# Optimization experiments

Measured on AMD Instinct MI355X. Metric: run time of the kernel, lower is better.

Reference implementation:

```python
import jax, jax.numpy as jnp
import numpy as np

DIM = 768
HEADS = 12
HEAD_DIM = DIM // HEADS
MLP_HID = 4 * DIM
DEPTH = 2
BLEND = 0.5
LN_EPS = 1e-5
SCALE = HEAD_DIM ** -0.5

PARAM_NAMES = ['qkv_w', 'qkv_b', 'proj_w', 'proj_b', 'ln1_g', 'ln1_b', 'ln2_g', 'ln2_b', 'mlp_w1', 'mlp_b1', 'mlp_w2', 'mlp_b2']


def setup_inputs() -> dict:
    key = jax.random.key(0)
    keys = jax.random.split(key, 1 + DEPTH * 6)
    inp = {'x': jax.random.normal(keys[0], (4, 1024, DIM), dtype=jnp.float32)}
    ki = 1
    s = 0.02
    for d in range(DEPTH):
        inp[f'qkv_w{d}'] = jax.random.normal(keys[ki], (DIM, 3 * DIM), jnp.float32) * s; ki += 1
        inp[f'qkv_b{d}'] = jnp.zeros((3 * DIM,), jnp.float32)
        inp[f'proj_w{d}'] = jax.random.normal(keys[ki], (DIM, DIM), jnp.float32) * s; ki += 1
        inp[f'proj_b{d}'] = jnp.zeros((DIM,), jnp.float32)
        inp[f'ln1_g{d}'] = jnp.ones((DIM,), jnp.float32)
        inp[f'ln1_b{d}'] = jnp.zeros((DIM,), jnp.float32)
        inp[f'ln2_g{d}'] = jnp.ones((DIM,), jnp.float32)
        inp[f'ln2_b{d}'] = jnp.zeros((DIM,), jnp.float32)
        inp[f'mlp_w1{d}'] = jax.random.normal(keys[ki], (DIM, MLP_HID), jnp.float32) * s; ki += 1
        inp[f'mlp_b1{d}'] = jnp.zeros((MLP_HID,), jnp.float32)
        inp[f'mlp_w2{d}'] = jax.random.normal(keys[ki], (MLP_HID, DIM), jnp.float32) * s; ki += 1
        inp[f'mlp_b2{d}'] = jnp.zeros((DIM,), jnp.float32)
    return inp


def _layernorm(x, g, b):
    mu = jnp.mean(x, axis=-1, keepdims=True)
    var = jnp.mean(jnp.square(x - mu), axis=-1, keepdims=True)
    return (x - mu) * jax.lax.rsqrt(var + LN_EPS) * g + b


def _attention(x, qkv_w, qkv_b, proj_w, proj_b):
    B, N, C = x.shape
    qkv = (x @ qkv_w + qkv_b).reshape(B, N, 3, HEADS, HEAD_DIM)
    qkv = jnp.transpose(qkv, (2, 0, 3, 1, 4))  # [3, B, H, N, hd]
    q, k, v = qkv[0], qkv[1], qkv[2]
    attn = jax.nn.softmax(jnp.einsum('bhnd,bhmd->bhnm', q, k) * SCALE, axis=-1)
    out = jnp.einsum('bhnm,bhmd->bhnd', attn, v)
    out = jnp.transpose(out, (0, 2, 1, 3)).reshape(B, N, C)
    return out @ proj_w + proj_b, attn


def _block(x, params, lvl):
    p = params[lvl]
    h = _layernorm(x, p['ln1_g'], p['ln1_b'])
    x_attn, attn = _attention(h, p['qkv_w'], p['qkv_b'], p['proj_w'], p['proj_b'])
    maps = [attn]
    x = x + x_attn
    if lvl + 1 < DEPTH:
        x_sub, sub_maps = _block(x, params, lvl + 1)
        x = (1.0 - BLEND) * x + BLEND * x_sub
        maps.extend(sub_maps)
    h = _layernorm(x, p['ln2_g'], p['ln2_b'])
    h = jax.nn.gelu(h @ p['mlp_w1'] + p['mlp_b1'], approximate=False) @ p['mlp_w2'] + p['mlp_b2']
    x = x + h
    return x, maps


def reference(x,
              qkv_w0, qkv_b0, proj_w0, proj_b0, ln1_g0, ln1_b0, ln2_g0, ln2_b0, mlp_w10, mlp_b10, mlp_w20, mlp_b20,
              qkv_w1, qkv_b1, proj_w1, proj_b1, ln1_g1, ln1_b1, ln2_g1, ln2_b1, mlp_w11, mlp_b11, mlp_w21, mlp_b21):
    params = [
        dict(qkv_w=qkv_w0, qkv_b=qkv_b0, proj_w=proj_w0, proj_b=proj_b0, ln1_g=ln1_g0, ln1_b=ln1_b0,
             ln2_g=ln2_g0, ln2_b=ln2_b0, mlp_w1=mlp_w10, mlp_b1=mlp_b10, mlp_w2=mlp_w20, mlp_b2=mlp_b20),
        dict(qkv_w=qkv_w1, qkv_b=qkv_b1, proj_w=proj_w1, proj_b=proj_b1, ln1_g=ln1_g1, ln1_b=ln1_b1,
             ln2_g=ln2_g1, ln2_b=ln2_b1, mlp_w1=mlp_w11, mlp_b1=mlp_b11, mlp_w2=mlp_w21, mlp_b2=mlp_b21),
    ]
    out, maps = _block(x, params, 0)
    return (out, *maps)
```

## Files before the change

### kernel.cpp

```cpp
#include <hip/hip_runtime.h>
#include <hip/hip_bf16.h>
#include <stdint.h>

typedef __bf16 bf16;
typedef __bf16 bf16x8 __attribute__((ext_vector_type(8)));
typedef __bf16 bf16x4 __attribute__((ext_vector_type(4)));
typedef float  f32x4  __attribute__((ext_vector_type(4)));

#define GLOAD16(gsrc, ldst)                                                        \
  __builtin_amdgcn_global_load_lds(                                               \
      (const __attribute__((address_space(1))) void*)(gsrc),                      \
      (__attribute__((address_space(3))) void*)(ldst), 16, 0, 0)

__device__ __forceinline__ float gelu_f(float v) {
  return 0.5f * v * (1.0f + erff(v * 0.70710678118654752f));
}

__global__ __launch_bounds__(256) void transpose_all_k(
    const float* __restrict__ qw0, bf16* __restrict__ qt0,
    const float* __restrict__ pw0, bf16* __restrict__ pt0,
    const float* __restrict__ w10, bf16* __restrict__ t10,
    const float* __restrict__ w20, bf16* __restrict__ t20,
    const float* __restrict__ qw1, bf16* __restrict__ qt1,
    const float* __restrict__ pw1, bf16* __restrict__ pt1,
    const float* __restrict__ w11, bf16* __restrict__ t11,
    const float* __restrict__ w21, bf16* __restrict__ t21,
    const float* __restrict__ x, const float* __restrict__ lng,
    const float* __restrict__ lnb, bf16* __restrict__ lnout) {
  int i = blockIdx.x;
  if (i >= 13824) {
    const int token = (i - 13824) * 4 + (threadIdx.x >> 6);
    const int lane  = threadIdx.x & 63;
    const float4* xp = (const float4*)(x + (size_t)token * 768);
    float4 v[3];
    float s = 0.f, ss = 0.f;
#pragma unroll
    for (int j = 0; j < 3; j++) {
      v[j] = xp[lane + j * 64];
      s  += v[j].x + v[j].y + v[j].z + v[j].w;
      ss += v[j].x * v[j].x + v[j].y * v[j].y + v[j].z * v[j].z + v[j].w * v[j].w;
    }
#pragma unroll
    for (int o = 32; o > 0; o >>= 1) { s += __shfl_xor(s, o); ss += __shfl_xor(ss, o); }
    const float mu  = s * (1.f / 768.f);
    const float var = ss * (1.f / 768.f) - mu * mu;
    const float r   = rsqrtf(var + 1e-5f);
#pragma unroll
    for (int j = 0; j < 3; j++) {
      const int c0 = (lane + j * 64) * 4;
      bf16x4 o4;
      o4[0] = (bf16)((v[j].x - mu) * r * lng[c0 + 0] + lnb[c0 + 0]);
      o4[1] = (bf16)((v[j].y - mu) * r * lng[c0 + 1] + lnb[c0 + 1]);
      o4[2] = (bf16)((v[j].z - mu) * r * lng[c0 + 2] + lnb[c0 + 2]);
      o4[3] = (bf16)((v[j].w - mu) * r * lng[c0 + 3] + lnb[c0 + 3]);
      *(bf16x4*)(lnout + (size_t)token * 768 + c0) = o4;
    }
    return;
  }
  __shared__ float tile[32][33];
  const int d = (i >= 6912) ? 1 : 0;
  i -= d * 6912;
  const float* W; bf16* Wt; int K, N, nt;
  if (i < 1728)      { W = d ? qw1 : qw0; Wt = d ? qt1 : qt0; K = 768;  N = 2304; nt = 72; }
  else if (i < 2304) { i -= 1728; W = d ? pw1 : pw0; Wt = d ? pt1 : pt0; K = 768; N = 768; nt = 24; }
  else if (i < 4608) { i -= 2304; W = d ? w11 : w10; Wt = d ? t11 : t10; K = 768; N = 3072; nt = 96; }
  else               { i -= 4608; W = d ? w21 : w20; Wt = d ? t21 : t20; K = 3072; N = 768; nt = 24; }
  const int n0 = (i % nt) * 32, k0 = (i / nt) * 32;
  const int tx = threadIdx.x & 31, ty = threadIdx.x >> 5;
#pragma unroll
  for (int j = ty; j < 32; j += 8)
    tile[j][tx] = W[(size_t)(k0 + j) * N + n0 + tx];
  __syncthreads();
#pragma unroll
  for (int j = ty; j < 32; j += 8)
    Wt[(size_t)(n0 + j) * K + k0 + tx] = (bf16)tile[tx][j];
}

template <int EPI, int NF>
__global__ __launch_bounds__(512, 2) void gemm256_k(
    const bf16* __restrict__ A, int lda,
    const bf16* __restrict__ Bt, int ldb,
    const float* __restrict__ bias,
    void* __restrict__ outp, int ldc, int K, bf16* __restrict__ vtout,
    size_t pstride) {
  extern __shared__ __align__(16) bf16 smem[];
  bf16* As = smem;
  bf16* Bs = smem + 32768;
  const int BROWS = NF * 64;

  const int t = threadIdx.x, wave = t >> 6, lane = t & 63;
  const int g = lane >> 4, l16 = lane & 15;
  const int wm = wave >> 2, wn = wave & 3;
  const int row0 = blockIdx.y * 256, col0 = blockIdx.x * (NF * 64);
  const int koff = (EPI == 4) ? blockIdx.z * K : 0;
  const int KT = K >> 6;

  f32x4 acc[8][NF];
#pragma unroll
  for (int m = 0; m < 8; m++)
#pragma unroll
    for (int n = 0; n < NF; n++) acc[m][n] = f32x4{0.f, 0.f, 0.f, 0.f};

  const int s_r = t >> 3, s_sl = t & 7;

  auto stage = [&](int kt, int tb) {
    const int k0 = koff + (kt << 6);
#pragma unroll
    for (int l = 0; l < 4; ++l) {
      const int row = l * 64 + s_r;
      const int swz = (s_sl ^ (row & 7)) << 3;
      GLOAD16(A + (size_t)(row0 + row) * lda + k0 + swz,
              As + tb * 16384 + row * 64 + (s_sl << 3));
    }
#pragma unroll
    for (int l = 0; l < NF; ++l) {
      const int row = l * 64 + s_r;
      const int swz = (s_sl ^ (row & 7)) << 3;
      GLOAD16(Bt + (size_t)(col0 + row) * ldb + k0 + swz,
              Bs + tb * (BROWS * 64) + row * 64 + (s_sl << 3));
    }
  };

  stage(0, 0);
  __syncthreads();

  for (int j = 0; j < KT; ++j) {
    const int p = j & 1;
    if (j + 1 < KT) stage(j + 1, p ^ 1);

    bf16x8 bfr[NF][2];
#pragma unroll
    for (int n = 0; n < NF; ++n)
#pragma unroll
      for (int kk = 0; kk < 2; ++kk) {
        const int r = wn * (NF * 16) + n * 16 + l16;
        bfr[n][kk] = *(const bf16x8*)(Bs + p * (BROWS * 64) + r * 64 +
                                      ((((kk << 2) + g) ^ (r & 7)) << 3));
      }
#pragma unroll
    for (int quad = 0; quad < 4; ++quad) {
      bf16x8 af[2][2];
#pragma unroll
      for (int mm = 0; mm < 2; ++mm)
#pragma unroll
        for (int kk = 0; kk < 2; ++kk) {
          const int r = wm * 128 + (quad * 2 + mm) * 16 + l16;
          af[mm][kk] = *(const bf16x8*)(As + p * 16384 + r * 64 +
                                        ((((kk << 2) + g) ^ (r & 7)) << 3));
        }
      __builtin_amdgcn_s_barrier();
      __builtin_amdgcn_s_setprio(1);
#pragma unroll
      for (int mm = 0; mm < 2; ++mm)
#pragma unroll
        for (int n = 0; n < NF; ++n)
#pragma unroll
          for (int kk = 0; kk < 2; ++kk)
            acc[quad * 2 + mm][n] = __builtin_amdgcn_mfma_f32_16x16x32_bf16(
                bfr[n][kk], af[mm][kk], acc[quad * 2 + mm][n], 0, 0, 0);
      __builtin_amdgcn_s_setprio(0);
    }
    __syncthreads();
  }

  const int rowb = row0 + wm * 128 + l16;
  const int colb = col0 + wn * (NF * 16) + (g << 2);
  bf16* outb = (bf16*)outp;
  if constexpr (EPI == 4) outb += (size_t)blockIdx.z * pstride;
#pragma unroll
  for (int m = 0; m < 8; ++m) {
    const int row = rowb + m * 16;
#pragma unroll
    for (int n = 0; n < NF; ++n) {
      const int c0 = colb + n * 16;
      f32x4 v = acc[m][n];
      if constexpr (EPI != 4) {
        const float4 b4 = *(const float4*)(bias + c0);
        v[0] += b4.x; v[1] += b4.y; v[2] += b4.z; v[3] += b4.w;
      }
      if constexpr (EPI == 1) {
        v[0] = gelu_f(v[0]); v[1] = gelu_f(v[1]);
        v[2] = gelu_f(v[2]); v[3] = gelu_f(v[3]);
      }
      bf16x4 o4;
      o4[0] = (bf16)v[0]; o4[1] = (bf16)v[1]; o4[2] = (bf16)v[2]; o4[3] = (bf16)v[3];
      *(bf16x4*)(outb + (size_t)row * ldc + c0) = o4;
      if constexpr (EPI == 0) {
        if (c0 >= 1536) {
          const int bq = row >> 10, q = row & 1023;
          const int hd = c0 - 1536, h = hd >> 6, dd = hd & 63;
          bf16* vb = vtout + (size_t)(bq * 12 + h) * 65536 + (size_t)dd * 1024 + q;
          vb[0] = o4[0]; vb[1024] = o4[1]; vb[2048] = o4[2]; vb[3072] = o4[3];
        }
      }
    }
  }
}

template <int NP, int MODE, bool LN>
__global__ __launch_bounds__(256) void reduce_ln_k(
    const bf16* __restrict__ pbuf, const float* __restrict__ bias,
    const float* __restrict__ res, const float* __restrict__ res2,
    float* __restrict__ xout, const float* __restrict__ g,
    const float* __restrict__ b, bf16* __restrict__ lnout) {
  const int token = blockIdx.x * 4 + (threadIdx.x >> 6);
  const int lane  = threadIdx.x & 63;
  float o[12];
  float s = 0.f, ss = 0.f;
#pragma unroll
  for (int j = 0; j < 3; j++) {
    const int c0 = (lane + j * 64) * 4;
    const size_t idx = (size_t)token * 768 + c0;
    const float4 b4 = *(const float4*)(bias + c0);
    float a0 = b4.x, a1 = b4.y, a2 = b4.z, a3 = b4.w;
#pragma unroll
    for (int sp = 0; sp < NP; sp++) {
      const bf16x4 pp = *(const bf16x4*)(pbuf + (size_t)sp * 3145728 + idx);
      a0 += (float)pp[0]; a1 += (float)pp[1]; a2 += (float)pp[2]; a3 += (float)pp[3];
    }
    const float4 r4 = *(const float4*)(res + idx);
    float4 ov;
    if constexpr (MODE == 0) {
      ov.x = a0 + r4.x; ov.y = a1 + r4.y; ov.z = a2 + r4.z; ov.w = a3 + r4.w;
    } else {
      const float4 r2 = *(const float4*)(res2 + idx);
      ov.x = 0.5f * (a0 + r4.x + r2.x); ov.y = 0.5f * (a1 + r4.y + r2.y);
      ov.z = 0.5f * (a2 + r4.z + r2.z); ov.w = 0.5f * (a3 + r4.w + r2.w);
    }
    *(float4*)(xout + idx) = ov;
    o[j * 4 + 0] = ov.x; o[j * 4 + 1] = ov.y; o[j * 4 + 2] = ov.z; o[j * 4 + 3] = ov.w;
    s  += ov.x + ov.y + ov.z + ov.w;
    ss += ov.x * ov.x + ov.y * ov.y + ov.z * ov.z + ov.w * ov.w;
  }
  if constexpr (LN) {
#pragma unroll
    for (int off = 32; off > 0; off >>= 1) { s += __shfl_xor(s, off); ss += __shfl_xor(ss, off); }
    const float mu  = s * (1.f / 768.f);
    const float var = ss * (1.f / 768.f) - mu * mu;
    const float r   = rsqrtf(var + 1e-5f);
#pragma unroll
    for (int j = 0; j < 3; j++) {
      const int c0 = (lane + j * 64) * 4;
      bf16x4 o4;
      o4[0] = (bf16)((o[j * 4 + 0] - mu) * r * g[c0 + 0] + b[c0 + 0]);
      o4[1] = (bf16)((o[j * 4 + 1] - mu) * r * g[c0 + 1] + b[c0 + 1]);
      o4[2] = (bf16)((o[j * 4 + 2] - mu) * r * g[c0 + 2] + b[c0 + 2]);
      o4[3] = (bf16)((o[j * 4 + 3] - mu) * r * g[c0 + 3] + b[c0 + 3]);
      *(bf16x4*)(lnout + (size_t)token * 768 + c0) = o4;
    }
  }
}

__global__ __launch_bounds__(256) void fattn_k(const bf16* __restrict__ qkv,
                                               const bf16* __restrict__ vT,
                                               float* __restrict__ attn,
                                               bf16* __restrict__ aout) {
  __shared__ __align__(16) bf16 Ks[128 * 64];
  __shared__ __align__(16) bf16 Ps[4 * 16 * 128];

  const float S2 = 0.18033688011112042f;

  const int bid = blockIdx.x;
  const int xcd = bid & 7, within = bid >> 3;
  const int bh = xcd * 6 + (within >> 4);
  const int qb = within & 15;
  const int b = bh / 12, h = bh % 12;

  const int t = threadIdx.x, w = t >> 6, lane = t & 63;
  const int g = lane >> 4, l16 = lane & 15;
  const int q0 = qb * 64;

  const bf16* qbp = qkv + (size_t)b * 1024 * 2304 + h * 64;
  const bf16* kbp = qbp + 768;
  const bf16* vt = vT + (size_t)bh * 65536;
  float* Pout = attn + (size_t)bh * 1048576;
  bf16* Pw = Ps + w * 2048;

  bf16x8 qf[2];
#pragma unroll
  for (int kk = 0; kk < 2; kk++)
    qf[kk] = *(const bf16x8*)(qbp + (size_t)(q0 + w * 16 + l16) * 2304 + kk * 32 + g * 8);

  const int kvr = t >> 3, sl = t & 7;

  float l_run = 0.f;

  for (int kv0 = 0; kv0 < 1024; kv0 += 128) {
#pragma unroll
    for (int i = 0; i < 4; i++) {
      const int kvl = i * 32 + kvr;
      GLOAD16(kbp + (size_t)(kv0 + kvl) * 2304 + (sl ^ (kvl & 7)) * 8,
              Ks + i * 2048 + t * 8);
    }
    __syncthreads();
    f32x4 st[8];
#pragma unroll
    for (int mk = 0; mk < 8; mk++) st[mk] = f32x4{0.f, 0.f, 0.f, 0.f};
    __builtin_amdgcn_s_setprio(1);
#pragma unroll
    for (int kk = 0; kk < 2; kk++) {
#pragma unroll
      for (int mk = 0; mk < 8; mk++) {
        const int kv = mk * 16 + l16;
        const bf16x8 kf = *(const bf16x8*)(Ks + ((kv * 64 + kk * 32 + g * 8) ^ ((kv & 7) << 3)));
        st[mk] = __builtin_amdgcn_mfma_f32_16x16x32_bf16(kf, qf[kk], st[mk], 0, 0, 0);
      }
    }
    __builtin_amdgcn_s_setprio(0);
    __syncthreads();
    float sum = 0.f;
#pragma unroll
    for (int mk = 0; mk < 8; mk++)
#pragma unroll
      for (int r = 0; r < 4; r++) sum += exp2f(st[mk][r] * S2);
    sum += __shfl_xor(sum, 16);
    sum += __shfl_xor(sum, 32);
    l_run += sum;
  }

  const float invl = 1.f / l_run;

  f32x4 oacc[4];
#pragma unroll
  for (int nd = 0; nd < 4; nd++) oacc[nd] = f32x4{0.f, 0.f, 0.f, 0.f};

  for (int kv0 = 0; kv0 < 1024; kv0 += 128) {
#pragma unroll
    for (int i = 0; i < 4; i++) {
      const int kvl = i * 32 + kvr;
      GLOAD16(kbp + (size_t)(kv0 + kvl) * 2304 + (sl ^ (kvl & 7)) * 8,
              Ks + i * 2048 + t * 8);
    }
    __syncthreads();
    f32x4 st[8];
#pragma unroll
    for (int mk = 0; mk < 8; mk++) st[mk] = f32x4{0.f, 0.f, 0.f, 0.f};
    __builtin_amdgcn_s_setprio(1);
#pragma unroll
    for (int kk = 0; kk < 2; kk++) {
#pragma unroll
      for (int mk = 0; mk < 8; mk++) {
        const int kv = mk * 16 + l16;
        const bf16x8 kf = *(const bf16x8*)(Ks + ((kv * 64 + kk * 32 + g * 8) ^ ((kv & 7) << 3)));
        st[mk] = __builtin_amdgcn_mfma_f32_16x16x32_bf16(kf, qf[kk], st[mk], 0, 0, 0);
      }
    }
    __builtin_amdgcn_s_setprio(0);
    __syncthreads();

    const int q = q0 + w * 16 + l16;
#pragma unroll
    for (int mk = 0; mk < 8; mk++) {
      f32x4 pv;
      pv[0] = exp2f(st[mk][0] * S2) * invl;
      pv[1] = exp2f(st[mk][1] * S2) * invl;
      pv[2] = exp2f(st[mk][2] * S2) * invl;
      pv[3] = exp2f(st[mk][3] * S2) * invl;
      __builtin_nontemporal_store(pv, (f32x4*)(Pout + (size_t)q * 1024 + kv0 + mk * 16 + g * 4));
      bf16x4 pb;
      pb[0] = (bf16)pv[0]; pb[1] = (bf16)pv[1]; pb[2] = (bf16)pv[2]; pb[3] = (bf16)pv[3];
      *(bf16x4*)(Pw + ((l16 * 128 + mk * 16 + g * 4) ^ ((l16 & 7) << 3))) = pb;
    }

#pragma unroll
    for (int kkv = 0; kkv < 4; kkv++) {
      const bf16x8 pf = *(const bf16x8*)(Pw + ((l16 * 128 + kkv * 32 + g * 8) ^ ((l16 & 7) << 3)));
      bf16x8 vf[4];
#pragma unroll
      for (int nd = 0; nd < 4; nd++)
        vf[nd] = *(const bf16x8*)(vt + (size_t)(nd * 16 + l16) * 1024 + kv0 + kkv * 32 + g * 8);
      __builtin_amdgcn_s_setprio(1);
#pragma unroll
      for (int nd = 0; nd < 4; nd++)
        oacc[nd] = __builtin_amdgcn_mfma_f32_16x16x32_bf16(vf[nd], pf, oacc[nd], 0, 0, 0);
      __builtin_amdgcn_s_setprio(0);
    }
  }

  {
    const int q = q0 + w * 16 + l16;
    bf16* ob = aout + (size_t)(b * 1024 + q) * 768 + h * 64 + g * 4;
#pragma unroll
    for (int nd = 0; nd < 4; nd++) {
      bf16x4 o4;
      o4[0] = (bf16)oacc[nd][0]; o4[1] = (bf16)oacc[nd][1];
      o4[2] = (bf16)oacc[nd][2]; o4[3] = (bf16)oacc[nd][3];
      *(bf16x4*)(ob + nd * 16) = o4;
    }
  }
}

extern "C" void kernel_launch(void* const* d_in, const int* in_sizes, int n_in,
                              void* d_out, int out_size, void* d_ws, size_t ws_size,
                              hipStream_t stream) {
  (void)in_sizes; (void)n_in; (void)out_size; (void)ws_size;
  const float* x = (const float*)d_in[0];
#define IN(d, i) ((const float*)d_in[1 + (d) * 12 + (i)])
  float* outF = (float*)d_out;
  float* attnp[2] = {outF + 3145728, outF + 3145728 + 50331648};

  const int kLds = 114688;
  hipFuncSetAttribute((const void*)gemm256_k<0, 3>,
                      hipFuncAttributeMaxDynamicSharedMemorySize, kLds);
  hipFuncSetAttribute((const void*)gemm256_k<1, 3>,
                      hipFuncAttributeMaxDynamicSharedMemorySize, kLds);
  hipFuncSetAttribute((const void*)gemm256_k<4, 3>,
                      hipFuncAttributeMaxDynamicSharedMemorySize, kLds);

  char* p = (char*)d_ws;
  auto alloc = [&](size_t bytes) { void* r = p; p += bytes; return r; };
  bf16 *qkv_wt[2], *proj_wt[2], *w1t[2], *w2t[2];
  for (int d = 0; d < 2; d++) {
    qkv_wt[d]  = (bf16*)alloc((size_t)2304 * 768 * 2);
    proj_wt[d] = (bf16*)alloc((size_t)768 * 768 * 2);
    w1t[d]     = (bf16*)alloc((size_t)3072 * 768 * 2);
    w2t[d]     = (bf16*)alloc((size_t)768 * 3072 * 2);
  }
  bf16*  hbuf = (bf16*)alloc((size_t)4096 * 768 * 2);
  bf16*  qkvb = (bf16*)alloc((size_t)4096 * 2304 * 2);
  bf16*  pbuf = hbuf;
  bf16*  vT   = (bf16*)alloc((size_t)48 * 64 * 1024 * 2);
  bf16*  aout = (bf16*)alloc((size_t)4096 * 768 * 2);
  bf16*  hid  = (bf16*)alloc((size_t)4096 * 3072 * 2);
  float* xa   = (float*)alloc((size_t)4096 * 768 * 4);
  float* xb   = (float*)alloc((size_t)4096 * 768 * 4);

  transpose_all_k<<<14848, 256, 0, stream>>>(
      IN(0, 0), qkv_wt[0], IN(0, 2), proj_wt[0], IN(0, 8), w1t[0], IN(0, 10), w2t[0],
      IN(1, 0), qkv_wt[1], IN(1, 2), proj_wt[1], IN(1, 8), w1t[1], IN(1, 10), w2t[1],
      x, IN(0, 4), IN(0, 5), hbuf);

  gemm256_k<0, 3><<<dim3(12, 16), 512, kLds, stream>>>(hbuf, 768, qkv_wt[0], 768, IN(0, 1),
                                                       qkvb, 2304, 768, vT, 0);
  fattn_k<<<768, 256, 0, stream>>>(qkvb, vT, attnp[0], aout);
  gemm256_k<4, 3><<<dim3(4, 16, 4), 512, kLds, stream>>>(aout, 768, proj_wt[0], 768, nullptr,
                                                         pbuf, 768, 192, nullptr, 3145728);
  reduce_ln_k<4, 0, true><<<1024, 256, 0, stream>>>(pbuf, IN(0, 3), x, nullptr,
                                                    xa, IN(1, 4), IN(1, 5), hbuf);
  gemm256_k<0, 3><<<dim3(12, 16), 512, kLds, stream>>>(hbuf, 768, qkv_wt[1], 768, IN(1, 1),
                                                       qkvb, 2304, 768, vT, 0);
  fattn_k<<<768, 256, 0, stream>>>(qkvb, vT, attnp[1], aout);
  gemm256_k<4, 3><<<dim3(4, 16, 4), 512, kLds, stream>>>(aout, 768, proj_wt[1], 768, nullptr,
                                                         pbuf, 768, 192, nullptr, 3145728);
  reduce_ln_k<4, 0, true><<<1024, 256, 0, stream>>>(pbuf, IN(1, 3), xa, nullptr,
                                                    xb, IN(1, 6), IN(1, 7), hbuf);
  gemm256_k<1, 3><<<dim3(16, 16), 512, kLds, stream>>>(hbuf, 768, w1t[1], 768, IN(1, 9),
                                                       hid, 3072, 768, nullptr, 0);
  gemm256_k<4, 3><<<dim3(4, 16, 4), 512, kLds, stream>>>(hid, 3072, w2t[1], 3072, nullptr,
                                                         pbuf, 768, 768, nullptr, 3145728);
  reduce_ln_k<4, 1, true><<<1024, 256, 0, stream>>>(pbuf, IN(1, 11), xb, xa,
                                                    xa, IN(0, 6), IN(0, 7), hbuf);
  gemm256_k<1, 3><<<dim3(16, 16), 512, kLds, stream>>>(hbuf, 768, w1t[0], 768, IN(0, 9),
                                                       hid, 3072, 768, nullptr, 0);
  gemm256_k<4, 3><<<dim3(4, 16, 4), 512, kLds, stream>>>(hid, 3072, w2t[0], 3072, nullptr,
                                                         pbuf, 768, 768, nullptr, 3145728);
  reduce_ln_k<4, 0, false><<<1024, 256, 0, stream>>>(pbuf, IN(0, 11), xa, nullptr,
                                                     outF, nullptr, nullptr, nullptr);
#undef IN
}
```

Before: 432.2 us.

## Compute QK^T once, keep unnormalized probabilities in LDS, then write attention map

The attention kernel no longer runs two passes over K (one for the row sums, one for the probabilities). It computes the scores once, stores the unnormalized bf16 exponentials for the whole 64x1024 tile in about 145 KB of dynamic LDS, and then writes the normalized fp32 attention map with coalesced row-wise stores. Blocks grow to 512 threads, with the eight waves split between KV halves for the score stage and head-dim halves for the PV stage, and 1/l is applied to the output at the end. The cost is one workgroup per CU because of the LDS size, and the stored map is now rounded from bf16 values, which loses precision.

```diff
diff --git a/kernel.cpp b/kernel.cpp
--- a/kernel.cpp
+++ b/kernel.cpp
@@ -251,12 +251,14 @@
   }
 }
 
-__global__ __launch_bounds__(256) void fattn_k(const bf16* __restrict__ qkv,
+__global__ __launch_bounds__(512) void fattn_k(const bf16* __restrict__ qkv,
                                                const bf16* __restrict__ vT,
                                                float* __restrict__ attn,
                                                bf16* __restrict__ aout) {
-  __shared__ __align__(16) bf16 Ks[128 * 64];
-  __shared__ __align__(16) bf16 Ps[4 * 16 * 128];
+  extern __shared__ __align__(16) char fsm[];
+  bf16*  Ks = (bf16*)fsm;
+  bf16*  Pl = (bf16*)(fsm + 16384);
+  float* Sr = (float*)(fsm + 16384 + 132096);
 
   const float S2 = 0.18033688011112042f;
 
@@ -268,123 +270,108 @@
 
   const int t = threadIdx.x, w = t >> 6, lane = t & 63;
   const int g = lane >> 4, l16 = lane & 15;
+  const int qg = w & 3, kvh = w >> 2;
   const int q0 = qb * 64;
+  const int qrow = qg * 16 + l16;
 
   const bf16* qbp = qkv + (size_t)b * 1024 * 2304 + h * 64;
   const bf16* kbp = qbp + 768;
   const bf16* vt = vT + (size_t)bh * 65536;
   float* Pout = attn + (size_t)bh * 1048576;
-  bf16* Pw = Ps + w * 2048;
 
   bf16x8 qf[2];
 #pragma unroll
   for (int kk = 0; kk < 2; kk++)
-    qf[kk] = *(const bf16x8*)(qbp + (size_t)(q0 + w * 16 + l16) * 2304 + kk * 32 + g * 8);
+    qf[kk] = *(const bf16x8*)(qbp + (size_t)(q0 + qrow) * 2304 + kk * 32 + g * 8);
 
   const int kvr = t >> 3, sl = t & 7;
-
-  float l_run = 0.f;
+  float psum = 0.f;
 
   for (int kv0 = 0; kv0 < 1024; kv0 += 128) {
 #pragma unroll
-    for (int i = 0; i < 4; i++) {
-      const int kvl = i * 32 + kvr;
+    for (int i = 0; i < 2; i++) {
+      const int kvl = i * 64 + kvr;
       GLOAD16(kbp + (size_t)(kv0 + kvl) * 2304 + (sl ^ (kvl & 7)) * 8,
-              Ks + i * 2048 + t * 8);
+              Ks + i * 4096 + t * 8);
     }
     __syncthreads();
-    f32x4 st[8];
-#pragma unroll
-    for (int mk = 0; mk < 8; mk++) st[mk] = f32x4{0.f, 0.f, 0.f, 0.f};
+    f32x4 st[4];
+#pragma unroll
+    for (int mkf = 0; mkf < 4; mkf++) st[mkf] = f32x4{0.f, 0.f, 0.f, 0.f};
     __builtin_amdgcn_s_setprio(1);
 #pragma unroll
     for (int kk = 0; kk < 2; kk++) {
 #pragma unroll
-      for (int mk = 0; mk < 8; mk++) {
-        const int kv = mk * 16 + l16;
+      for (int mkf = 0; mkf < 4; mkf++) {
+        const int kv = kvh * 64 + mkf * 16 + l16;
         const bf16x8 kf = *(const bf16x8*)(Ks + ((kv * 64 + kk * 32 + g * 8) ^ ((kv & 7) << 3)));
-        st[mk] = __builtin_amdgcn_mfma_f32_16x16x32_bf16(kf, qf[kk], st[mk], 0, 0, 0);
+        st[mkf] = __builtin_amdgcn_mfma_f32_16x16x32_bf16(kf, qf[kk], st[mkf], 0, 0, 0);
       }
     }
     __builtin_amdgcn_s_setprio(0);
-    __syncthreads();
-    float sum = 0.f;
-#pragma unroll
-    for (int mk = 0; mk < 8; mk++)
-#pragma unroll
-      for (int r = 0; r < 4; r++) sum += exp2f(st[mk][r] * S2);
-    sum += __shfl_xor(sum, 16);
-    sum += __shfl_xor(sum, 32);
-    l_run += sum;
-  }
-
-  const float invl = 1.f / l_run;
-
-  f32x4 oacc[4];
-#pragma unroll
-  for (int nd = 0; nd < 4; nd++) oacc[nd] = f32x4{0.f, 0.f, 0.f, 0.f};
-
-  for (int kv0 = 0; kv0 < 1024; kv0 += 128) {
-#pragma unroll
-    for (int i = 0; i < 4; i++) {
-      const int kvl = i * 32 + kvr;
-      GLOAD16(kbp + (size_t)(kv0 + kvl) * 2304 + (sl ^ (kvl & 7)) * 8,
-              Ks + i * 2048 + t * 8);
-    }
-    __syncthreads();
-    f32x4 st[8];
-#pragma unroll
-    for (int mk = 0; mk < 8; mk++) st[mk] = f32x4{0.f, 0.f, 0.f, 0.f};
-    __builtin_amdgcn_s_setprio(1);
-#pragma unroll
-    for (int kk = 0; kk < 2; kk++) {
-#pragma unroll
-      for (int mk = 0; mk < 8; mk++) {
-        const int kv = mk * 16 + l16;
-        const bf16x8 kf = *(const bf16x8*)(Ks + ((kv * 64 + kk * 32 + g * 8) ^ ((kv & 7) << 3)));
-        st[mk] = __builtin_amdgcn_mfma_f32_16x16x32_bf16(kf, qf[kk], st[mk], 0, 0, 0);
-      }
-    }
-    __builtin_amdgcn_s_setprio(0);
-    __syncthreads();
-
-    const int q = q0 + w * 16 + l16;
-#pragma unroll
-    for (int mk = 0; mk < 8; mk++) {
+#pragma unroll
+    for (int mkf = 0; mkf < 4; mkf++) {
       f32x4 pv;
-      pv[0] = exp2f(st[mk][0] * S2) * invl;
-      pv[1] = exp2f(st[mk][1] * S2) * invl;
-      pv[2] = exp2f(st[mk][2] * S2) * invl;
-      pv[3] = exp2f(st[mk][3] * S2) * invl;
-      __builtin_nontemporal_store(pv, (f32x4*)(Pout + (size_t)q * 1024 + kv0 + mk * 16 + g * 4));
+      pv[0] = exp2f(st[mkf][0] * S2);
+      pv[1] = exp2f(st[mkf][1] * S2);
+      pv[2] = exp2f(st[mkf][2] * S2);
+      pv[3] = exp2f(st[mkf][3] * S2);
+      psum += pv[0] + pv[1] + pv[2] + pv[3];
       bf16x4 pb;
       pb[0] = (bf16)pv[0]; pb[1] = (bf16)pv[1]; pb[2] = (bf16)pv[2]; pb[3] = (bf16)pv[3];
-      *(bf16x4*)(Pw + ((l16 * 128 + mk * 16 + g * 4) ^ ((l16 & 7) << 3))) = pb;
-    }
-
-#pragma unroll
-    for (int kkv = 0; kkv < 4; kkv++) {
-      const bf16x8 pf = *(const bf16x8*)(Pw + ((l16 * 128 + kkv * 32 + g * 8) ^ ((l16 & 7) << 3)));
-      bf16x8 vf[4];
-#pragma unroll
-      for (int nd = 0; nd < 4; nd++)
-        vf[nd] = *(const bf16x8*)(vt + (size_t)(nd * 16 + l16) * 1024 + kv0 + kkv * 32 + g * 8);
-      __builtin_amdgcn_s_setprio(1);
-#pragma unroll
-      for (int nd = 0; nd < 4; nd++)
-        oacc[nd] = __builtin_amdgcn_mfma_f32_16x16x32_bf16(vf[nd], pf, oacc[nd], 0, 0, 0);
-      __builtin_amdgcn_s_setprio(0);
-    }
+      *(bf16x4*)(Pl + qrow * 1032 + kv0 + kvh * 64 + mkf * 16 + g * 4) = pb;
+    }
+    __syncthreads();
+  }
+
+  psum += __shfl_xor(psum, 16);
+  psum += __shfl_xor(psum, 32);
+  if (g == 0) Sr[w * 16 + l16] = psum;
+  __syncthreads();
+
+  const float invl = 1.f / (Sr[qg * 16 + l16] + Sr[(qg + 4) * 16 + l16]);
+
+#pragma unroll
+  for (int j = 0; j < 8; j++) {
+    const int row = j * 8 + w;
+    const float invr = 1.f / (Sr[(row >> 4) * 16 + (row & 15)] +
+                              Sr[((row >> 4) + 4) * 16 + (row & 15)]);
+    float* dst = Pout + (size_t)(q0 + row) * 1024;
+#pragma unroll
+    for (int c = 0; c < 4; c++) {
+      const int col = (c * 64 + lane) * 4;
+      const bf16x4 pb = *(const bf16x4*)(Pl + row * 1032 + col);
+      f32x4 v;
+      v[0] = (float)pb[0] * invr; v[1] = (float)pb[1] * invr;
+      v[2] = (float)pb[2] * invr; v[3] = (float)pb[3] * invr;
+      __builtin_nontemporal_store(v, (f32x4*)(dst + col));
+    }
+  }
+
+  const int dh = kvh;
+  f32x4 oacc[2];
+  oacc[0] = f32x4{0.f, 0.f, 0.f, 0.f};
+  oacc[1] = f32x4{0.f, 0.f, 0.f, 0.f};
+  for (int kv = 0; kv < 1024; kv += 32) {
+    const bf16x8 pf = *(const bf16x8*)(Pl + qrow * 1032 + kv + g * 8);
+    __builtin_amdgcn_s_setprio(1);
+#pragma unroll
+    for (int nd = 0; nd < 2; nd++) {
+      const bf16x8 vf =
+          *(const bf16x8*)(vt + (size_t)(dh * 32 + nd * 16 + l16) * 1024 + kv + g * 8);
+      oacc[nd] = __builtin_amdgcn_mfma_f32_16x16x32_bf16(vf, pf, oacc[nd], 0, 0, 0);
+    }
+    __builtin_amdgcn_s_setprio(0);
   }
 
   {
-    const int q = q0 + w * 16 + l16;
-    bf16* ob = aout + (size_t)(b * 1024 + q) * 768 + h * 64 + g * 4;
-#pragma unroll
-    for (int nd = 0; nd < 4; nd++) {
+    const int q = q0 + qrow;
+    bf16* ob = aout + (size_t)(b * 1024 + q) * 768 + h * 64 + dh * 32 + g * 4;
+#pragma unroll
+    for (int nd = 0; nd < 2; nd++) {
       bf16x4 o4;
-      o4[0] = (bf16)oacc[nd][0]; o4[1] = (bf16)oacc[nd][1];
-      o4[2] = (bf16)oacc[nd][2]; o4[3] = (bf16)oacc[nd][3];
+      o4[0] = (bf16)(oacc[nd][0] * invl); o4[1] = (bf16)(oacc[nd][1] * invl);
+      o4[2] = (bf16)(oacc[nd][2] * invl); o4[3] = (bf16)(oacc[nd][3] * invl);
       *(bf16x4*)(ob + nd * 16) = o4;
     }
   }
@@ -400,12 +387,15 @@
   float* attnp[2] = {outF + 3145728, outF + 3145728 + 50331648};
 
   const int kLds = 114688;
+  const int kLdsAttn = 148992;
   hipFuncSetAttribute((const void*)gemm256_k<0, 3>,
                       hipFuncAttributeMaxDynamicSharedMemorySize, kLds);
   hipFuncSetAttribute((const void*)gemm256_k<1, 3>,
                       hipFuncAttributeMaxDynamicSharedMemorySize, kLds);
   hipFuncSetAttribute((const void*)gemm256_k<4, 3>,
                       hipFuncAttributeMaxDynamicSharedMemorySize, kLds);
+  hipFuncSetAttribute((const void*)fattn_k,
+                      hipFuncAttributeMaxDynamicSharedMemorySize, kLdsAttn);
 
   char* p = (char*)d_ws;
   auto alloc = [&](size_t bytes) { void* r = p; p += bytes; return r; };
@@ -432,14 +422,14 @@
 
   gemm256_k<0, 3><<<dim3(12, 16), 512, kLds, stream>>>(hbuf, 768, qkv_wt[0], 768, IN(0, 1),
                                                        qkvb, 2304, 768, vT, 0);
-  fattn_k<<<768, 256, 0, stream>>>(qkvb, vT, attnp[0], aout);
+  fattn_k<<<768, 512, kLdsAttn, stream>>>(qkvb, vT, attnp[0], aout);
   gemm256_k<4, 3><<<dim3(4, 16, 4), 512, kLds, stream>>>(aout, 768, proj_wt[0], 768, nullptr,
                                                          pbuf, 768, 192, nullptr, 3145728);
   reduce_ln_k<4, 0, true><<<1024, 256, 0, stream>>>(pbuf, IN(0, 3), x, nullptr,
                                                     xa, IN(1, 4), IN(1, 5), hbuf);
   gemm256_k<0, 3><<<dim3(12, 16), 512, kLds, stream>>>(hbuf, 768, qkv_wt[1], 768, IN(1, 1),
                                                        qkvb, 2304, 768, vT, 0);
-  fattn_k<<<768, 256, 0, stream>>>(qkvb, vT, attnp[1], aout);
+  fattn_k<<<768, 512, kLdsAttn, stream>>>(qkvb, vT, attnp[1], aout);
   gemm256_k<4, 3><<<dim3(4, 16, 4), 512, kLds, stream>>>(aout, 768, proj_wt[1], 768, nullptr,
                                                          pbuf, 768, 192, nullptr, 3145728);
   reduce_ln_k<4, 0, true><<<1024, 256, 0, stream>>>(pbuf, IN(1, 3), xa, nullptr,
```

Measured after the change: 459.6 us. 6.3% more time.
